# Performance work log

Measured on AMD Instinct MI355X. Metric: run time of the kernel, lower is better.

The kernel has to match this reference:

```python
import jax, jax.numpy as jnp
import numpy as np

N_NODES = 8      # 4 regions + 4 boundaries
N_STEPS = 3


def _step_graph(nodes, Wd, Ws, b):
    """One all-pairs message-passing step.

    nodes: [N, B, C, H, W]
    Wd:    [N, C, C]  receiver-i conv weight acting on (nodes[j] - nodes[i])
    Ws:    [N, C, C]  receiver-i conv weight acting on nodes[i]
    b:     [N, C]
    edges[j][i] = Wd_i @ (nodes[j]-nodes[i]) + Ws_i @ nodes[i] + b_i   (1x1 conv)
    out[i] = sum_{j != i} relu(edges[j][i]) * nodes[j] + nodes[i]
    """
    # receiver-dependent self term: [N(i), B, C, H, W]
    self_term = jnp.einsum('iod,ibdhw->ibohw', Ws, nodes) + b[:, None, :, None, None]
    # pairwise differences nodes[j] - nodes[i]: [N(j), N(i), B, C, H, W]
    diff = nodes[:, None] - nodes[None, :]
    e = jnp.einsum('iod,jibdhw->jibohw', Wd, diff) + self_term[None]
    gate = jax.nn.relu(e)
    # zero out the diagonal (i == j contributes nothing)
    mask = (1.0 - jnp.eye(N_NODES, dtype=nodes.dtype))[:, :, None, None, None, None]
    gate = gate * mask
    # message[i] = sum_j gate[j,i] * nodes[j]
    msg = jnp.einsum('jibchw,jbchw->ibchw', gate, nodes)
    return msg + nodes


def setup_inputs() -> dict:
    key = jax.random.key(0)
    k1, k2, k3 = jax.random.split(key, 3)
    B, C, H, W = 4, 32, 96, 96
    nodes = jax.random.normal(k1, (N_NODES, B, C, H, W), dtype=jnp.float32)
    # 1x1 conv weights [N, C_out, 2C_in]; scaled ~1/(2C) to keep 3 steps numerically tame
    W_edge = jax.random.normal(k2, (N_NODES, C, 2 * C), dtype=jnp.float32) * 0.05
    b_edge = jax.random.normal(k3, (N_NODES, C), dtype=jnp.float32) * 0.05
    return {"nodes": nodes, "W_edge": W_edge, "b_edge": b_edge}


def reference(nodes, W_edge, b_edge):
    C = nodes.shape[2]
    Wd = W_edge[:, :, :C]   # acts on nodes[j] - nodes[i]
    Ws = W_edge[:, :, C:]   # acts on nodes[i]
    for _ in range(N_STEPS):
        nodes = _step_graph(nodes, Wd, Ws, b_edge)
    return nodes  # [N, B, C, H, W]; first half = regions, second half = boundaries
```

## Files before the change

### kernel.cpp

```cpp
#include <hip/hip_runtime.h>
#include <hip/hip_bf16.h>


#define NN 8
#define NSTEPS 3
#define BB 4
#define CC 32
#define HWSZ 9216
#define PX 16
#define CPS 40
#define CPG 36
#define MSC 2048.0f
#define SINV 4.8828125e-4f

typedef _Float16 f16x8 __attribute__((ext_vector_type(8)));
typedef _Float16 f16x4 __attribute__((ext_vector_type(4)));
typedef _Float16 f16x2 __attribute__((ext_vector_type(2)));
typedef float    f32x4 __attribute__((ext_vector_type(4)));
typedef float    f32x2 __attribute__((ext_vector_type(2)));

#define MFMA(A, B, C) __builtin_amdgcn_mfma_f32_16x16x32_f16((A), (B), (C), 0, 0, 0)

__device__ __forceinline__ void split2s(float v, _Float16& h, _Float16& m) {
    h = (_Float16)v;
    m = (_Float16)((v - (float)h) * MSC);
}

__global__ __launch_bounds__(256, 2)
void gcn3_f16(const float* __restrict__ nodes,
              const float* __restrict__ we,
              const float* __restrict__ be,
              float* __restrict__ out) {
    __shared__ _Float16 xs[2][NN][PX][CPS];
    __shared__ float    xg[NN][PX][CPG];

    const int tid  = threadIdx.x;
    const int wid  = tid >> 6;
    const int lane = tid & 63;
    const int col  = lane & 15;
    const int quad = lane >> 4;

    const f32x4 zero4 = {0.f, 0.f, 0.f, 0.f};

    f16x8 awd[2][2][2], awsd[2][2][2];
    f32x4 bias[2][2];
    #pragma unroll
    for (int r = 0; r < 2; ++r) {
        const int ir = wid + 4 * r;
        #pragma unroll
        for (int t = 0; t < 2; ++t) {
            const float* wp = we + (size_t)((ir * CC + 16 * t + col) * (2 * CC)) + quad * 8;
            f32x4 d0 = *(const f32x4*)wp;
            f32x4 d1 = *(const f32x4*)(wp + 4);
            f32x4 s0 = *(const f32x4*)(wp + CC);
            f32x4 s1 = *(const f32x4*)(wp + CC + 4);
            #pragma unroll
            for (int k = 0; k < 8; ++k) {
                float d = (k < 4) ? d0[k & 3] : d1[k & 3];
                float s = (k < 4) ? s0[k & 3] : s1[k & 3];
                _Float16 h, m;
                split2s(d, h, m);
                awd[r][t][0][k] = h; awd[r][t][1][k] = m;
                split2s(s - d, h, m);
                awsd[r][t][0][k] = h; awsd[r][t][1][k] = m;
            }
            #pragma unroll
            for (int k = 0; k < 4; ++k)
                bias[r][t][k] = be[ir * CC + 16 * t + quad * 4 + k];
        }
    }

    const int q0  = blockIdx.x * PX;
    const int b   = q0 / HWSZ;
    const int hw0 = q0 - b * HWSZ;

    #pragma unroll
    for (int kk = 0; kk < 4; ++kk) {
        int idx = tid + kk * 256;
        int p2 = (idx & 7) * 2;
        int c2 = ((idx >> 3) & 15) * 2;
        int n  = idx >> 7;
        const float* gp = nodes + (size_t)((n * BB + b) * CC + c2) * HWSZ + hw0 + p2;
        f32x2 v0 = *(const f32x2*)gp;
        f32x2 v1 = *(const f32x2*)(gp + HWSZ);
        #pragma unroll
        for (int e = 0; e < 2; ++e) {
            _Float16 h0, m0, h1, m1;
            split2s(v0[e], h0, m0);
            split2s(v1[e], h1, m1);
            *(f16x2*)&xs[0][n][p2 + e][c2] = f16x2{h0, h1};
            *(f16x2*)&xs[1][n][p2 + e][c2] = f16x2{m0, m1};
            *(f32x2*)&xg[n][p2 + e][c2] = f32x2{v0[e], v1[e]};
        }
    }
    __syncthreads();

    f32x4 msg[2][2];

    #pragma unroll 1
    for (int step = 0; step < NSTEPS; ++step) {
        f32x4 qf[2][2];
        #pragma unroll
        for (int r = 0; r < 2; ++r) {
            const int ir = wid + 4 * r;
            f16x8 bh = *(const f16x8*)&xs[0][ir][col][quad * 8];
            f16x8 bm = *(const f16x8*)&xs[1][ir][col][quad * 8];
            #pragma unroll
            for (int t = 0; t < 2; ++t) {
                f32x4 q1 = MFMA(awsd[r][t][0], bh, bias[r][t]);
                f32x4 q2 = MFMA(awsd[r][t][0], bm, zero4);
                q2 = MFMA(awsd[r][t][1], bh, q2);
                f32x4 q3 = MFMA(awsd[r][t][1], bm, zero4);
                #pragma unroll
                for (int k = 0; k < 4; ++k)
                    qf[r][t][k] = fmaf(fmaf(q3[k], SINV, q2[k]), SINV, q1[k]);
            }
        }

        #pragma unroll
        for (int r = 0; r < 2; ++r)
            #pragma unroll
            for (int t = 0; t < 2; ++t)
                msg[r][t] = zero4;

        #pragma unroll
        for (int j = 0; j < NN; ++j) {
            f16x8 bh = *(const f16x8*)&xs[0][j][col][quad * 8];
            f16x8 bm = *(const f16x8*)&xs[1][j][col][quad * 8];
            f32x4 xgj[2];
            #pragma unroll
            for (int t = 0; t < 2; ++t)
                xgj[t] = *(const f32x4*)&xg[j][col][16 * t + quad * 4];
            #pragma unroll
            for (int r = 0; r < 2; ++r) {
                if (j == wid + 4 * r) {
                    #pragma unroll
                    for (int t = 0; t < 2; ++t)
                        #pragma unroll
                        for (int k = 0; k < 4; ++k)
                            msg[r][t][k] += xgj[t][k];
                } else {
                    #pragma unroll
                    for (int t = 0; t < 2; ++t) {
                        f32x4 e1 = MFMA(awd[r][t][0], bh, qf[r][t]);
                        f32x4 e2 = MFMA(awd[r][t][0], bm, zero4);
                        e2 = MFMA(awd[r][t][1], bh, e2);
                        #pragma unroll
                        for (int k = 0; k < 4; ++k) {
                            float g = fmaxf(fmaf(e2[k], SINV, e1[k]), 0.f);
                            msg[r][t][k] = fmaf(g, xgj[t][k], msg[r][t][k]);
                        }
                    }
                }
            }
        }

        if (step < NSTEPS - 1) {
            __syncthreads();
            #pragma unroll
            for (int r = 0; r < 2; ++r) {
                const int ir = wid + 4 * r;
                #pragma unroll
                for (int t = 0; t < 2; ++t) {
                    f16x4 h4, m4;
                    #pragma unroll
                    for (int k = 0; k < 4; ++k) {
                        _Float16 h, m;
                        split2s(msg[r][t][k], h, m);
                        h4[k] = h; m4[k] = m;
                    }
                    *(f16x4*)&xs[0][ir][col][16 * t + quad * 4] = h4;
                    *(f16x4*)&xs[1][ir][col][16 * t + quad * 4] = m4;
                    *(f32x4*)&xg[ir][col][16 * t + quad * 4] = msg[r][t];
                }
            }
            __syncthreads();
        }
    }

    __syncthreads();
    #pragma unroll
    for (int r = 0; r < 2; ++r) {
        const int ir = wid + 4 * r;
        #pragma unroll
        for (int t = 0; t < 2; ++t)
            *(f32x4*)&xg[ir][col][16 * t + quad * 4] = msg[r][t];
    }
    __syncthreads();
    #pragma unroll
    for (int kk = 0; kk < 4; ++kk) {
        int idx = tid + kk * 256;
        int p4 = (idx & 3) * 4;
        int c  = (idx >> 2) & 31;
        int n  = idx >> 7;
        f32x4 v;
        #pragma unroll
        for (int e = 0; e < 4; ++e) v[e] = xg[n][p4 + e][c];
        *(f32x4*)(out + (size_t)((n * BB + b) * CC + c) * HWSZ + hw0 + p4) = v;
    }
}

extern "C" void kernel_launch(void* const* d_in, const int* in_sizes, int n_in,
                              void* d_out, int out_size, void* d_ws, size_t ws_size,
                              hipStream_t stream) {
    const float* nodes  = (const float*)d_in[0];
    const float* W_edge = (const float*)d_in[1];
    const float* b_edge = (const float*)d_in[2];
    float* outp = (float*)d_out;

    dim3 grid((BB * HWSZ) / PX);
    dim3 block(256);
    gcn3_f16<<<grid, block, 0, stream>>>(nodes, W_edge, b_edge, outp);
}
```

Baseline: 136.4 us.

## Use one wave per receiver node with 512-thread blocks

Doubles the block to 8 waves so each wave owns a single receiver node instead of two. This halves per-wave weight registers and MFMA chains and raises the occupancy target through launch bounds of 512 threads with 4 blocks. The B-operand LDS loads for sender j now happen only on off-diagonal iterations. The cost is more waves contending at the barriers, and each wave loses the reuse of its loaded node data across two receivers.

```diff
diff --git a/kernel.cpp b/kernel.cpp
--- a/kernel.cpp
+++ b/kernel.cpp
@@ -26,11 +26,11 @@
     m = (_Float16)((v - (float)h) * MSC);
 }
 
-__global__ __launch_bounds__(256, 2)
-void gcn3_f16(const float* __restrict__ nodes,
-              const float* __restrict__ we,
-              const float* __restrict__ be,
-              float* __restrict__ out) {
+__global__ __launch_bounds__(512, 4)
+void gcn3_f16w(const float* __restrict__ nodes,
+               const float* __restrict__ we,
+               const float* __restrict__ be,
+               float* __restrict__ out) {
     __shared__ _Float16 xs[2][NN][PX][CPS];
     __shared__ float    xg[NN][PX][CPG];
 
@@ -42,32 +42,28 @@
 
     const f32x4 zero4 = {0.f, 0.f, 0.f, 0.f};
 
-    f16x8 awd[2][2][2], awsd[2][2][2];
-    f32x4 bias[2][2];
+    f16x8 awd[2][2], awsd[2][2];
+    f32x4 bias[2];
     #pragma unroll
-    for (int r = 0; r < 2; ++r) {
-        const int ir = wid + 4 * r;
+    for (int t = 0; t < 2; ++t) {
+        const float* wp = we + (size_t)((wid * CC + 16 * t + col) * (2 * CC)) + quad * 8;
+        f32x4 d0 = *(const f32x4*)wp;
+        f32x4 d1 = *(const f32x4*)(wp + 4);
+        f32x4 s0 = *(const f32x4*)(wp + CC);
+        f32x4 s1 = *(const f32x4*)(wp + CC + 4);
         #pragma unroll
-        for (int t = 0; t < 2; ++t) {
-            const float* wp = we + (size_t)((ir * CC + 16 * t + col) * (2 * CC)) + quad * 8;
-            f32x4 d0 = *(const f32x4*)wp;
-            f32x4 d1 = *(const f32x4*)(wp + 4);
-            f32x4 s0 = *(const f32x4*)(wp + CC);
-            f32x4 s1 = *(const f32x4*)(wp + CC + 4);
-            #pragma unroll
-            for (int k = 0; k < 8; ++k) {
-                float d = (k < 4) ? d0[k & 3] : d1[k & 3];
-                float s = (k < 4) ? s0[k & 3] : s1[k & 3];
-                _Float16 h, m;
-                split2s(d, h, m);
-                awd[r][t][0][k] = h; awd[r][t][1][k] = m;
-                split2s(s - d, h, m);
-                awsd[r][t][0][k] = h; awsd[r][t][1][k] = m;
-            }
-            #pragma unroll
-            for (int k = 0; k < 4; ++k)
-                bias[r][t][k] = be[ir * CC + 16 * t + quad * 4 + k];
+        for (int k = 0; k < 8; ++k) {
+            float d = (k < 4) ? d0[k & 3] : d1[k & 3];
+            float s = (k < 4) ? s0[k & 3] : s1[k & 3];
+            _Float16 h, m;
+            split2s(d, h, m);
+            awd[t][0][k] = h; awd[t][1][k] = m;
+            split2s(s - d, h, m);
+            awsd[t][0][k] = h; awsd[t][1][k] = m;
         }
+        #pragma unroll
+        for (int k = 0; k < 4; ++k)
+            bias[t][k] = be[wid * CC + 16 * t + quad * 4 + k];
     }
 
     const int q0  = blockIdx.x * PX;
@@ -75,8 +71,8 @@
     const int hw0 = q0 - b * HWSZ;
 
     #pragma unroll
-    for (int kk = 0; kk < 4; ++kk) {
-        int idx = tid + kk * 256;
+    for (int kk = 0; kk < 2; ++kk) {
+        int idx = tid + kk * 512;
         int p2 = (idx & 7) * 2;
         int c2 = ((idx >> 3) & 15) * 2;
         int n  = idx >> 7;
@@ -95,61 +91,54 @@
     }
     __syncthreads();
 
-    f32x4 msg[2][2];
+    f32x4 msg[2];
 
     #pragma unroll 1
     for (int step = 0; step < NSTEPS; ++step) {
-        f32x4 qf[2][2];
-        #pragma unroll
-        for (int r = 0; r < 2; ++r) {
-            const int ir = wid + 4 * r;
-            f16x8 bh = *(const f16x8*)&xs[0][ir][col][quad * 8];
-            f16x8 bm = *(const f16x8*)&xs[1][ir][col][quad * 8];
+        f32x4 qf[2];
+        {
+            f16x8 bh = *(const f16x8*)&xs[0][wid][col][quad * 8];
+            f16x8 bm = *(const f16x8*)&xs[1][wid][col][quad * 8];
             #pragma unroll
             for (int t = 0; t < 2; ++t) {
-                f32x4 q1 = MFMA(awsd[r][t][0], bh, bias[r][t]);
-                f32x4 q2 = MFMA(awsd[r][t][0], bm, zero4);
-                q2 = MFMA(awsd[r][t][1], bh, q2);
-                f32x4 q3 = MFMA(awsd[r][t][1], bm, zero4);
+                f32x4 q1 = MFMA(awsd[t][0], bh, bias[t]);
+                f32x4 q2 = MFMA(awsd[t][0], bm, zero4);
+                q2 = MFMA(awsd[t][1], bh, q2);
+                f32x4 q3 = MFMA(awsd[t][1], bm, zero4);
                 #pragma unroll
                 for (int k = 0; k < 4; ++k)
-                    qf[r][t][k] = fmaf(fmaf(q3[k], SINV, q2[k]), SINV, q1[k]);
+                    qf[t][k] = fmaf(fmaf(q3[k], SINV, q2[k]), SINV, q1[k]);
             }
         }
 
         #pragma unroll
-        for (int r = 0; r < 2; ++r)
-            #pragma unroll
-            for (int t = 0; t < 2; ++t)
-                msg[r][t] = zero4;
+        for (int t = 0; t < 2; ++t)
+            msg[t] = zero4;
 
         #pragma unroll
         for (int j = 0; j < NN; ++j) {
-            f16x8 bh = *(const f16x8*)&xs[0][j][col][quad * 8];
-            f16x8 bm = *(const f16x8*)&xs[1][j][col][quad * 8];
             f32x4 xgj[2];
             #pragma unroll
             for (int t = 0; t < 2; ++t)
                 xgj[t] = *(const f32x4*)&xg[j][col][16 * t + quad * 4];
-            #pragma unroll
-            for (int r = 0; r < 2; ++r) {
-                if (j == wid + 4 * r) {
+            if (j == wid) {
+                #pragma unroll
+                for (int t = 0; t < 2; ++t)
                     #pragma unroll
-                    for (int t = 0; t < 2; ++t)
-                        #pragma unroll
-                        for (int k = 0; k < 4; ++k)
-                            msg[r][t][k] += xgj[t][k];
-                } else {
+                    for (int k = 0; k < 4; ++k)
+                        msg[t][k] += xgj[t][k];
+            } else {
+                f16x8 bh = *(const f16x8*)&xs[0][j][col][quad * 8];
+                f16x8 bm = *(const f16x8*)&xs[1][j][col][quad * 8];
+                #pragma unroll
+                for (int t = 0; t < 2; ++t) {
+                    f32x4 e1 = MFMA(awd[t][0], bh, qf[t]);
+                    f32x4 e2 = MFMA(awd[t][0], bm, zero4);
+                    e2 = MFMA(awd[t][1], bh, e2);
                     #pragma unroll
-                    for (int t = 0; t < 2; ++t) {
-                        f32x4 e1 = MFMA(awd[r][t][0], bh, qf[r][t]);
-                        f32x4 e2 = MFMA(awd[r][t][0], bm, zero4);
-                        e2 = MFMA(awd[r][t][1], bh, e2);
-                        #pragma unroll
-                        for (int k = 0; k < 4; ++k) {
-                            float g = fmaxf(fmaf(e2[k], SINV, e1[k]), 0.f);
-                            msg[r][t][k] = fmaf(g, xgj[t][k], msg[r][t][k]);
-                        }
+                    for (int k = 0; k < 4; ++k) {
+                        float g = fmaxf(fmaf(e2[k], SINV, e1[k]), 0.f);
+                        msg[t][k] = fmaf(g, xgj[t][k], msg[t][k]);
                     }
                 }
             }
@@ -158,21 +147,17 @@
         if (step < NSTEPS - 1) {
             __syncthreads();
             #pragma unroll
-            for (int r = 0; r < 2; ++r) {
-                const int ir = wid + 4 * r;
+            for (int t = 0; t < 2; ++t) {
+                f16x4 h4, m4;
                 #pragma unroll
-                for (int t = 0; t < 2; ++t) {
-                    f16x4 h4, m4;
-                    #pragma unroll
-                    for (int k = 0; k < 4; ++k) {
-                        _Float16 h, m;
-                        split2s(msg[r][t][k], h, m);
-                        h4[k] = h; m4[k] = m;
-                    }
-                    *(f16x4*)&xs[0][ir][col][16 * t + quad * 4] = h4;
-                    *(f16x4*)&xs[1][ir][col][16 * t + quad * 4] = m4;
-                    *(f32x4*)&xg[ir][col][16 * t + quad * 4] = msg[r][t];
+                for (int k = 0; k < 4; ++k) {
+                    _Float16 h, m;
+                    split2s(msg[t][k], h, m);
+                    h4[k] = h; m4[k] = m;
                 }
+                *(f16x4*)&xs[0][wid][col][16 * t + quad * 4] = h4;
+                *(f16x4*)&xs[1][wid][col][16 * t + quad * 4] = m4;
+                *(f32x4*)&xg[wid][col][16 * t + quad * 4] = msg[t];
             }
             __syncthreads();
         }
@@ -180,16 +165,12 @@
 
     __syncthreads();
     #pragma unroll
-    for (int r = 0; r < 2; ++r) {
-        const int ir = wid + 4 * r;
-        #pragma unroll
-        for (int t = 0; t < 2; ++t)
-            *(f32x4*)&xg[ir][col][16 * t + quad * 4] = msg[r][t];
-    }
+    for (int t = 0; t < 2; ++t)
+        *(f32x4*)&xg[wid][col][16 * t + quad * 4] = msg[t];
     __syncthreads();
     #pragma unroll
-    for (int kk = 0; kk < 4; ++kk) {
-        int idx = tid + kk * 256;
+    for (int kk = 0; kk < 2; ++kk) {
+        int idx = tid + kk * 512;
         int p4 = (idx & 3) * 4;
         int c  = (idx >> 2) & 31;
         int n  = idx >> 7;
@@ -209,6 +190,6 @@
     float* outp = (float*)d_out;
 
     dim3 grid((BB * HWSZ) / PX);
-    dim3 block(256);
-    gcn3_f16<<<grid, block, 0, stream>>>(nodes, W_edge, b_edge, outp);
+    dim3 block(512);
+    gcn3_f16w<<<grid, block, 0, stream>>>(nodes, W_edge, b_edge, outp);
 }
```

Measured after the change: 131.9 us. -3.3%, faster.
